# Performance work log

Hardware: AMD Instinct MI355X
Metric: run time of the kernel (lower is better)

The kernel has to match this reference:

```python
import jax, jax.numpy as jnp
import numpy as np

DIM = 2560
HEADS = 64
HEAD_DIM = 40
TEMB = 512
FF = 4 * DIM
B = 1
S = 1248
TXT = 224
EPS = 1e-6


def _ln(x, eps=EPS):
    # LayerNorm over last dim, no affine (elementwise_affine=False)
    m = jnp.mean(x, axis=-1, keepdims=True)
    v = jnp.mean(jnp.square(x - m), axis=-1, keepdims=True)
    return (x - m) * jax.lax.rsqrt(v + eps)


def setup_inputs() -> dict:
    key = jax.random.key(0)
    ks = jax.random.split(key, 10)
    w = 0.02
    return {
        "hidden_states": jax.random.normal(ks[0], (B, S, DIM), jnp.float32),
        "emb": jax.random.normal(ks[1], (B, TEMB), jnp.float32),
        "attention_mask": jnp.zeros((B, 1, S, S), jnp.float32),
        "adaln_w": jax.random.normal(ks[2], (TEMB, 12 * DIM), jnp.float32) * w,
        "adaln_b": jnp.zeros((12 * DIM,), jnp.float32),
        "qkv_w": jax.random.normal(ks[3], (DIM, 3 * DIM), jnp.float32) * w,
        "qkv_b": jnp.zeros((3 * DIM,), jnp.float32),
        "out_w": jax.random.normal(ks[4], (DIM, DIM), jnp.float32) * w,
        "out_b": jnp.zeros((DIM,), jnp.float32),
        "ff1_w": jax.random.normal(ks[5], (DIM, FF), jnp.float32) * w,
        "ff1_b": jnp.zeros((FF,), jnp.float32),
        "ff2_w": jax.random.normal(ks[6], (FF, DIM), jnp.float32) * w,
        "ff2_b": jnp.zeros((DIM,), jnp.float32),
        "text_length": TXT,
    }


def reference(hidden_states, emb, attention_mask, adaln_w, adaln_b, qkv_w, qkv_b,
              out_w, out_b, ff1_w, ff1_b, ff2_w, ff2_b, text_length):
    b, s, d = hidden_states.shape
    t = text_length

    # adaLN: SiLU -> Linear(time_embed_dim, 12*dim), chunk into 12 [B, dim] pieces
    ada = jax.nn.silu(emb) @ adaln_w + adaln_b
    (sh_msa_i, sc_msa_i, g_msa_i, sh_mlp_i, sc_mlp_i, g_mlp_i,
     sh_msa_t, sc_msa_t, g_msa_t, sh_mlp_t, sc_mlp_t, g_mlp_t) = jnp.split(ada, 12, axis=1)

    def mod(x, shift, scale):
        return x * (1.0 + scale[:, None, :]) + shift[:, None, :]

    # --- attention block ---
    ai = _ln(hidden_states)
    ai = jnp.concatenate([mod(ai[:, :t], sh_msa_t, sc_msa_t),
                          mod(ai[:, t:], sh_msa_i, sc_msa_i)], axis=1)

    qkv = ai @ qkv_w + qkv_b                              # [B, S, 3*D]
    q, k, v = jnp.split(qkv, 3, axis=-1)
    q = q.reshape(b, s, HEADS, HEAD_DIM).transpose(0, 2, 1, 3)  # [B, H, S, hd]
    k = k.reshape(b, s, HEADS, HEAD_DIM).transpose(0, 2, 1, 3)
    v = v.reshape(b, s, HEADS, HEAD_DIM).transpose(0, 2, 1, 3)

    q = _ln(q)  # per-head QK layernorm
    k = _ln(k)

    scores = jnp.einsum("bhqd,bhkd->bhqk", q, k) / (HEAD_DIM ** 0.5)
    scores = scores + attention_mask
    probs = jax.nn.softmax(scores, axis=-1)
    ctx = jnp.einsum("bhqk,bhkd->bhqd", probs, v)
    ctx = ctx.transpose(0, 2, 1, 3).reshape(b, s, d)
    attn_out = ctx @ out_w + out_b

    h = jnp.concatenate([hidden_states[:, :t] + g_msa_t[:, None, :] * attn_out[:, :t],
                         hidden_states[:, t:] + g_msa_i[:, None, :] * attn_out[:, t:]], axis=1)

    # --- MLP block ---
    mi = _ln(h)
    mi = jnp.concatenate([mod(mi[:, :t], sh_mlp_t, sc_mlp_t),
                          mod(mi[:, t:], sh_mlp_i, sc_mlp_i)], axis=1)
    mo = jax.nn.gelu(mi @ ff1_w + ff1_b, approximate=True) @ ff2_w + ff2_b

    h = jnp.concatenate([h[:, :t] + g_mlp_t[:, None, :] * mo[:, :t],
                         h[:, t:] + g_mlp_i[:, None, :] * mo[:, t:]], axis=1)
    return h
```

## Files before the change

### kernel.cpp

```cpp
#include <hip/hip_runtime.h>
#include <cstdint>

typedef float f32x4 __attribute__((ext_vector_type(4)));
typedef __bf16 bf16x8 __attribute__((ext_vector_type(8)));
typedef __bf16 bf16x4 __attribute__((ext_vector_type(4)));

#define S_LEN 1248
#define S_PAD 1280
#define DIMD 2560
#define NHEAD 64
#define HDIM 40
#define T3 7680

__device__ __forceinline__ f32x4 mfma16(bf16x8 a, bf16x8 b, f32x4 c) {
  return __builtin_amdgcn_mfma_f32_16x16x32_bf16(a, b, c, 0, 0, 0);
}

__global__ void k_adaln(const float* __restrict__ emb, const float* __restrict__ W,
                        const float* __restrict__ b, float* __restrict__ ada) {
  __shared__ __attribute__((aligned(16))) float se[512];
  int tid = threadIdx.x;
  for (int i = tid; i < 512; i += 64) {
    float e = emb[i];
    se[i] = e / (1.f + __expf(-e));
  }
  __syncthreads();
  int col = blockIdx.x * 64 + tid;
  float acc = 0.f;
  #pragma unroll 8
  for (int k = 0; k < 512; ++k) acc += se[k] * W[(size_t)k * 30720 + col];
  ada[col] = acc + b[col];
}

__global__ __launch_bounds__(256) void k_trans(const float* __restrict__ W,
                                               __bf16* __restrict__ Wt, int K, int N) {
  __shared__ __attribute__((aligned(16))) float t[64][65];
  int k0 = blockIdx.y * 64, n0 = blockIdx.x * 64;
  int tid = threadIdx.x;
  #pragma unroll
  for (int i = 0; i < 4; ++i) {
    int r = i * 16 + (tid >> 4), c = (tid & 15) * 4;
    const float4 v = *(const float4*)&W[(size_t)(k0 + r) * N + n0 + c];
    t[r][c] = v.x; t[r][c + 1] = v.y; t[r][c + 2] = v.z; t[r][c + 3] = v.w;
  }
  __syncthreads();
  #pragma unroll
  for (int j = 0; j < 4; ++j) {
    int n = j * 16 + (tid >> 4), kk = (tid & 15) * 4;
    bf16x4 o;
    o[0] = (__bf16)t[kk][n];     o[1] = (__bf16)t[kk + 1][n];
    o[2] = (__bf16)t[kk + 2][n]; o[3] = (__bf16)t[kk + 3][n];
    *(bf16x4*)&Wt[(size_t)(n0 + n) * K + k0 + kk] = o;
  }
}

__global__ __launch_bounds__(256) void k_lnmod(const float* __restrict__ X,
                                               const float* __restrict__ ada,
                                               int csh_t, int csc_t, int csh_i, int csc_i,
                                               const int* __restrict__ tlp,
                                               __bf16* __restrict__ Y) {
  int row = blockIdx.x, tid = threadIdx.x;
  const float* x = X + (size_t)row * DIMD;
  float v[10], s = 0.f, s2 = 0.f;
  #pragma unroll
  for (int i = 0; i < 10; ++i) { v[i] = x[tid + i * 256]; s += v[i]; s2 += v[i] * v[i]; }
  #pragma unroll
  for (int m = 1; m < 64; m <<= 1) { s += __shfl_xor(s, m, 64); s2 += __shfl_xor(s2, m, 64); }
  __shared__ float rs[4], rq[4];
  if ((tid & 63) == 0) { rs[tid >> 6] = s; rq[tid >> 6] = s2; }
  __syncthreads();
  s = rs[0] + rs[1] + rs[2] + rs[3];
  s2 = rq[0] + rq[1] + rq[2] + rq[3];
  float mean = s * (1.f / DIMD);
  float rstd = rsqrtf(s2 * (1.f / DIMD) - mean * mean + 1e-6f);
  int txt = *tlp;
  int csh = row < txt ? csh_t : csh_i, csc = row < txt ? csc_t : csc_i;
  #pragma unroll
  for (int i = 0; i < 10; ++i) {
    int col = tid + i * 256;
    float y = (v[i] - mean) * rstd;
    y = y * (1.f + ada[csc * DIMD + col]) + ada[csh * DIMD + col];
    Y[(size_t)row * DIMD + col] = (__bf16)y;
  }
}

template <int EPI>
__global__ __launch_bounds__(256) void k_gemm(
    const __bf16* __restrict__ A, int lda, const __bf16* __restrict__ Bt, int ldb,
    const float* __restrict__ bias, int N, int ksize,
    float* __restrict__ Cf, float* __restrict__ Cp, __bf16* __restrict__ Cb) {
  __shared__ __attribute__((aligned(16))) __bf16 smem[3][2][4096];
  int tid = threadIdx.x;

  unsigned gx = gridDim.x, gy = gridDim.y;
  unsigned nwg = gx * gy * gridDim.z;
  unsigned orig = (blockIdx.z * gy + blockIdx.y) * gx + blockIdx.x;
  unsigned qq = nwg >> 3, r8 = nwg & 7;
  unsigned xcd = orig & 7, loc = orig >> 3;
  unsigned swz = (xcd < r8 ? xcd * (qq + 1) : r8 * (qq + 1) + (xcd - r8) * qq) + loc;
  unsigned bx = swz % gx;
  unsigned rest = swz / gx;
  unsigned by = rest % gy;
  unsigned bz = rest / gy;

  int m0 = bx * 128, n0 = by * 128;
  int kbase = bz * ksize;
  int wave = tid >> 6, lane = tid & 63;
  int wm = (wave & 1) * 64, wn = (wave >> 1) * 64;
  int l15 = lane & 15, l4 = lane >> 4;
  f32x4 acc[4][4] = {};

  auto STG = [&](__bf16* As, __bf16* Bs, int kk) {
    #pragma unroll
    for (int i = 0; i < 2; ++i) {
      int c = tid + i * 256;
      int row = c >> 2, ko = (c & 3) * 8;
      __builtin_amdgcn_global_load_lds(
          (const __attribute__((address_space(1))) unsigned int*)(A + (size_t)(m0 + row) * lda + kk + ko),
          (__attribute__((address_space(3))) unsigned int*)(As + c * 8), 16, 0, 0);
      __builtin_amdgcn_global_load_lds(
          (const __attribute__((address_space(1))) unsigned int*)(Bt + (size_t)(n0 + row) * ldb + kk + ko),
          (__attribute__((address_space(3))) unsigned int*)(Bs + c * 8), 16, 0, 0);
    }
  };

  int nt = ksize >> 5;
  STG(smem[0][0], smem[0][1], kbase);
  STG(smem[1][0], smem[1][1], kbase + 32);
  asm volatile("s_waitcnt vmcnt(4)" ::: "memory");
  __builtin_amdgcn_s_barrier();

  int rb = 0, sb = 2;
  for (int t = 0; t < nt; ++t) {
    if (t + 2 < nt) STG(smem[sb][0], smem[sb][1], kbase + (t + 2) * 32);
    const __bf16* As = smem[rb][0];
    const __bf16* Bs = smem[rb][1];
    bf16x8 af[4], bfr[4];
    #pragma unroll
    for (int s = 0; s < 4; ++s) {
      af[s] = *(const bf16x8*)&As[(wm + s * 16 + l15) * 32 + l4 * 8];
      bfr[s] = *(const bf16x8*)&Bs[(wn + s * 16 + l15) * 32 + l4 * 8];
    }
    __builtin_amdgcn_s_setprio(1);
    #pragma unroll
    for (int i = 0; i < 4; ++i)
      #pragma unroll
      for (int j = 0; j < 4; ++j)
        acc[i][j] = mfma16(af[i], bfr[j], acc[i][j]);
    __builtin_amdgcn_s_setprio(0);
    __builtin_amdgcn_sched_barrier(0);
    if (t + 2 < nt)
      asm volatile("s_waitcnt vmcnt(4)" ::: "memory");
    else
      asm volatile("s_waitcnt vmcnt(0)" ::: "memory");
    __builtin_amdgcn_s_barrier();
    rb = rb == 2 ? 0 : rb + 1;
    sb = sb == 2 ? 0 : sb + 1;
  }

  float* Cfo = Cf;
  if constexpr (EPI == 3) Cfo = (bz == 0) ? Cf : (Cp + (size_t)(bz - 1) * S_PAD * N);
  #pragma unroll
  for (int i = 0; i < 4; ++i) {
    #pragma unroll
    for (int r = 0; r < 4; ++r) {
      int rr = m0 + wm + i * 16 + l4 * 4 + r;
      if (rr >= S_LEN) continue;
      #pragma unroll
      for (int j = 0; j < 4; ++j) {
        int col = n0 + wn + j * 16 + l15;
        if constexpr (EPI == 0) {
          Cfo[(size_t)rr * N + col] = acc[i][j][r] + bias[col];
        } else if constexpr (EPI == 3) {
          Cfo[(size_t)rr * N + col] = acc[i][j][r];
        } else if constexpr (EPI == 4) {
          Cb[(size_t)rr * N + col] = (__bf16)(acc[i][j][r] + bias[col]);
        } else {
          float val = acc[i][j][r] + bias[col];
          float u = val + 0.044715f * val * val * val;
          float gl = 0.5f * val * (1.f + tanhf(0.7978845608028654f * u));
          Cb[(size_t)rr * N + col] = (__bf16)gl;
        }
      }
    }
  }
}

template <int NS>
__global__ __launch_bounds__(256) void k_red(const float* __restrict__ p0,
                                             const float* __restrict__ prest,
                                             const float* __restrict__ bias,
                                             const float* __restrict__ resid,
                                             const float* __restrict__ ada,
                                             int g_t, int g_i, const int* __restrict__ tlp,
                                             int N, float* __restrict__ out) {
  int idx = blockIdx.x * 256 + threadIdx.x;
  int perRow = N >> 2;
  int row = idx / perRow;
  int c4 = (idx - row * perRow) << 2;
  if (row >= S_LEN) return;
  int txt = *tlp;
  size_t off = (size_t)row * N + c4;
  float4 s = *(const float4*)&p0[off];
  #pragma unroll
  for (int z = 0; z < NS - 1; ++z) {
    const float4 p = *(const float4*)&prest[(size_t)z * S_PAD * N + off];
    s.x += p.x; s.y += p.y; s.z += p.z; s.w += p.w;
  }
  const float4 bb = *(const float4*)&bias[c4];
  const float4 rr = *(const float4*)&resid[off];
  const float4 gg = *(const float4*)&ada[(size_t)(row < txt ? g_t : g_i) * DIMD + c4];
  float4 o;
  o.x = rr.x + gg.x * (s.x + bb.x);
  o.y = rr.y + gg.y * (s.y + bb.y);
  o.z = rr.z + gg.z * (s.z + bb.z);
  o.w = rr.w + gg.w * (s.w + bb.w);
  *(float4*)&out[off] = o;
}

__global__ __launch_bounds__(128) void k_qkln(const __bf16* __restrict__ qkv,
                                              __bf16* __restrict__ Qb, __bf16* __restrict__ Kb) {
  __shared__ __attribute__((aligned(16))) float buf[5120];
  int srow = blockIdx.x, tid = threadIdx.x;
  const __bf16* rowp = qkv + (size_t)srow * T3;
  for (int i = tid; i < 640; i += 128) {
    bf16x8 v = *(const bf16x8*)&rowp[i * 8];
    #pragma unroll
    for (int j = 0; j < 8; ++j) buf[i * 8 + j] = (float)v[j];
  }
  __syncthreads();
  int h = tid & 63;
  bool isK = tid >= 64;
  const float* x = buf + (isK ? DIMD : 0) + h * HDIM;
  float xv[40], s = 0.f;
  #pragma unroll
  for (int d = 0; d < 40; ++d) { xv[d] = x[d]; s += xv[d]; }
  float mean = s * (1.f / 40.f);
  float s2 = 0.f;
  #pragma unroll
  for (int d = 0; d < 40; ++d) { float t = xv[d] - mean; s2 += t * t; }
  float rstd = rsqrtf(s2 * (1.f / 40.f) + 1e-6f);
  float scale = isK ? rstd : rstd * 0.15811388300841897f;
  __bf16* dst = (isK ? Kb : Qb) + ((size_t)h * S_PAD + srow) * 64;
  #pragma unroll
  for (int i = 0; i < 5; ++i) {
    bf16x8 w;
    #pragma unroll
    for (int j = 0; j < 8; ++j) w[j] = (__bf16)((xv[i * 8 + j] - mean) * scale);
    *(bf16x8*)&dst[i * 8] = w;
  }
  bf16x8 z = {};
  *(bf16x8*)&dst[40] = z;
  *(bf16x8*)&dst[48] = z;
  *(bf16x8*)&dst[56] = z;
}

__global__ __launch_bounds__(256) void k_vtrans(const __bf16* __restrict__ qkv,
                                                __bf16* __restrict__ Vt) {
  __shared__ __attribute__((aligned(16))) float t[64][41];
  int h = blockIdx.y, s0 = blockIdx.x * 64;
  int tid = threadIdx.x;
  for (int i = tid; i < 64 * 40; i += 256) {
    int sr = i / 40, d = i - sr * 40;
    int srow = s0 + sr;
    t[sr][d] = (srow < S_LEN) ? (float)qkv[(size_t)srow * T3 + 2 * DIMD + h * HDIM + d] : 0.f;
  }
  __syncthreads();
  int d = tid >> 2, sc = (tid & 3) * 16;
  bf16x8 w0 = {}, w1 = {};
  if (d < 40) {
    #pragma unroll
    for (int q = 0; q < 8; ++q) {
      w0[q] = (__bf16)t[sc + q][d];
      w1[q] = (__bf16)t[sc + 8 + q][d];
    }
  } else if (d == 40) {
    #pragma unroll
    for (int q = 0; q < 8; ++q) { w0[q] = (__bf16)1.0f; w1[q] = (__bf16)1.0f; }
  }
  __bf16* dst = Vt + ((size_t)h * 64 + d) * S_PAD + s0 + sc;
  *(bf16x8*)&dst[0] = w0;
  *(bf16x8*)&dst[8] = w1;
}

__global__ __launch_bounds__(256) void k_attn(const __bf16* __restrict__ Qb,
                                              const __bf16* __restrict__ Kb,
                                              const __bf16* __restrict__ Vt,
                                              const float* __restrict__ mask,
                                              __bf16* __restrict__ ctx) {
  __shared__ __attribute__((aligned(16))) __bf16 kvs[2][2][4096];
  __shared__ __attribute__((aligned(16))) __bf16 plds[4][2][1024];
  unsigned orig = blockIdx.y * 10 + blockIdx.x;
  unsigned swz = (orig & 7) * 80 + (orig >> 3);
  int h = swz / 10, q0 = (swz % 10) * 128;
  int tid = threadIdx.x, wave = tid >> 6, lane = tid & 63;
  int l15 = lane & 15, l4 = lane >> 4;
  int qb = q0 + wave * 32;

  const __bf16* Kh = Kb + (size_t)h * S_PAD * 64;
  const __bf16* Vh = Vt + (size_t)h * 64 * S_PAD;

  auto STAGE = [&](int buf, int kv0) {
    #pragma unroll
    for (int i = 0; i < 2; ++i) {
      int c = tid + i * 256;
      int row = c >> 3, col = ((c & 7) ^ (row & 7)) * 8;
      __builtin_amdgcn_global_load_lds(
          (const __attribute__((address_space(1))) unsigned int*)(Kh + (size_t)(kv0 + row) * 64 + col),
          (__attribute__((address_space(3))) unsigned int*)&kvs[buf][0][c * 8], 16, 0, 0);
      __builtin_amdgcn_global_load_lds(
          (const __attribute__((address_space(1))) unsigned int*)(Vh + (size_t)row * S_PAD + kv0 + col),
          (__attribute__((address_space(3))) unsigned int*)&kvs[buf][1][c * 8], 16, 0, 0);
    }
  };

  bf16x8 qf[2][2];
  #pragma unroll
  for (int g = 0; g < 2; ++g) {
    const __bf16* Qp = Qb + ((size_t)h * S_PAD + qb + g * 16 + l15) * 64 + l4 * 8;
    qf[g][0] = *(const bf16x8*)Qp;
    qf[g][1] = *(const bf16x8*)(Qp + 32);
  }
  const float* mrow[2][4];
  #pragma unroll
  for (int g = 0; g < 2; ++g)
    #pragma unroll
    for (int r = 0; r < 4; ++r) {
      int qr = qb + g * 16 + l4 * 4 + r;
      mrow[g][r] = mask + (size_t)(qr < S_LEN ? qr : S_LEN - 1) * S_LEN;
    }
  f32x4 o[2][3] = {};

  STAGE(0, 0);
  for (int t = 0; t < 20; ++t) {
    int kv0 = t * 64;
    if (t < 19) {
      STAGE((t + 1) & 1, kv0 + 64);
      asm volatile("s_waitcnt vmcnt(4)" ::: "memory");
    } else {
      asm volatile("s_waitcnt vmcnt(0)" ::: "memory");
    }
    __builtin_amdgcn_s_barrier();
    const __bf16* Ks = kvs[t & 1][0];
    const __bf16* Vs = kvs[t & 1][1];

    float mreg[2][4][4];
    #pragma unroll
    for (int g = 0; g < 2; ++g)
      #pragma unroll
      for (int ns = 0; ns < 4; ++ns) {
        int kvc = kv0 + ns * 16 + l15;
        int mc = kvc < S_LEN ? kvc : S_LEN - 1;
        #pragma unroll
        for (int r = 0; r < 4; ++r) mreg[g][ns][r] = mrow[g][r][mc];
      }

    bf16x8 kf[4][2];
    #pragma unroll
    for (int ns = 0; ns < 4; ++ns) {
      int kvr = ns * 16 + l15, sw = kvr & 7;
      kf[ns][0] = *(const bf16x8*)((const char*)Ks + kvr * 128 + ((l4 ^ sw) << 4));
      kf[ns][1] = *(const bf16x8*)((const char*)Ks + kvr * 128 + (((4 + l4) ^ sw) << 4));
    }
    bf16x8 vf[3][2];
    #pragma unroll
    for (int d3 = 0; d3 < 3; ++d3) {
      int dr = d3 * 16 + l15, sw = dr & 7;
      vf[d3][0] = *(const bf16x8*)((const char*)Vs + dr * 128 + ((l4 ^ sw) << 4));
      vf[d3][1] = *(const bf16x8*)((const char*)Vs + dr * 128 + (((4 + l4) ^ sw) << 4));
    }

    #pragma unroll
    for (int g = 0; g < 2; ++g) {
      f32x4 sf[4];
      #pragma unroll
      for (int ns = 0; ns < 4; ++ns) {
        f32x4 a = {};
        a = mfma16(qf[g][0], kf[ns][0], a);
        a = mfma16(qf[g][1], kf[ns][1], a);
        sf[ns] = a;
      }
      #pragma unroll
      for (int ns = 0; ns < 4; ++ns) {
        int kvc = kv0 + ns * 16 + l15;
        #pragma unroll
        for (int r = 0; r < 4; ++r) {
          float val = sf[ns][r] - 8.f + mreg[g][ns][r];
          if (kvc >= S_LEN) val = -100.f;
          float e = __expf(val);
          int prow = l4 * 4 + r;
          int boff = (prow * 128 + (ns * 16 + l15) * 2) ^ ((prow & 7) << 4);
          plds[wave][g][boff >> 1] = (__bf16)e;
        }
      }
      int swp = (l15 & 7) << 4;
      int ba = l15 * 128 + l4 * 16;
      bf16x8 pa0 = *(const bf16x8*)((const char*)plds[wave][g] + (ba ^ swp));
      bf16x8 pa1 = *(const bf16x8*)((const char*)plds[wave][g] + ((ba + 64) ^ swp));
      #pragma unroll
      for (int d3 = 0; d3 < 3; ++d3) {
        o[g][d3] = mfma16(pa0, vf[d3][0], o[g][d3]);
        o[g][d3] = mfma16(pa1, vf[d3][1], o[g][d3]);
      }
    }
    __builtin_amdgcn_s_barrier();
  }

  #pragma unroll
  for (int g = 0; g < 2; ++g) {
    #pragma unroll
    for (int r = 0; r < 4; ++r) {
      float sum = __shfl(o[g][2][r], (lane & 0x30) + 8, 64);
      float rinv = 1.f / sum;
      int qr = qb + g * 16 + l4 * 4 + r;
      if (qr < S_LEN) {
        #pragma unroll
        for (int d3 = 0; d3 < 3; ++d3) {
          int d = d3 * 16 + l15;
          if (d < HDIM)
            ctx[(size_t)qr * DIMD + h * HDIM + d] = (__bf16)(o[g][d3][r] * rinv);
        }
      }
    }
  }
}

extern "C" void kernel_launch(void* const* d_in, const int* in_sizes, int n_in,
                              void* d_out, int out_size, void* d_ws, size_t ws_size,
                              hipStream_t stream) {
  const float* hidden  = (const float*)d_in[0];
  const float* emb     = (const float*)d_in[1];
  const float* mask    = (const float*)d_in[2];
  const float* adaln_w = (const float*)d_in[3];
  const float* adaln_b = (const float*)d_in[4];
  const float* qkv_w   = (const float*)d_in[5];
  const float* qkv_b   = (const float*)d_in[6];
  const float* out_w   = (const float*)d_in[7];
  const float* out_b   = (const float*)d_in[8];
  const float* ff1_w   = (const float*)d_in[9];
  const float* ff1_b   = (const float*)d_in[10];
  const float* ff2_w   = (const float*)d_in[11];
  const float* ff2_b   = (const float*)d_in[12];
  const int*   tl      = (const int*)d_in[13];
  (void)in_sizes; (void)n_in; (void)out_size; (void)ws_size;

  char* w = (char*)d_ws;
  size_t off = 0;
  auto alloc = [&](size_t b) { char* p = w + off; off += (b + 255) & ~(size_t)255; return p; };
  float*  ada  = (float*)alloc(30720 * 4);
  __bf16* wT   = (__bf16*)alloc((size_t)10240 * 2560 * 2);
  __bf16* ai   = (__bf16*)alloc((size_t)S_PAD * DIMD * 2);
  __bf16* actB = (__bf16*)alloc((size_t)S_PAD * 10240 * 2);
  __bf16* Qb   = (__bf16*)alloc((size_t)NHEAD * S_PAD * 64 * 2);
  __bf16* Kb   = (__bf16*)alloc((size_t)NHEAD * S_PAD * 64 * 2);
  __bf16* Vt   = (__bf16*)alloc((size_t)NHEAD * 64 * S_PAD * 2);
  __bf16* ctxb = (__bf16*)alloc((size_t)S_PAD * DIMD * 2);
  float*  hbuf = (float*)alloc((size_t)S_PAD * DIMD * 4);
  __bf16* mi    = ai;
  __bf16* qkvB  = actB;
  __bf16* ff1o  = actB;
  float*  partO = (float*)Qb;
  float*  partF = (float*)Qb;

  k_adaln<<<dim3(480), dim3(64), 0, stream>>>(emb, adaln_w, adaln_b, ada);
  k_lnmod<<<dim3(1248), dim3(256), 0, stream>>>(hidden, ada, 6, 7, 0, 1, tl, ai);
  k_trans<<<dim3(7680 / 64, 2560 / 64), dim3(256), 0, stream>>>(qkv_w, wT, 2560, 7680);
  k_gemm<4><<<dim3(10, 60, 1), dim3(256), 0, stream>>>(ai, 2560, wT, 2560, qkv_b, 7680, 2560,
                                                       nullptr, nullptr, qkvB);
  k_qkln<<<dim3(1248), dim3(128), 0, stream>>>(qkvB, Qb, Kb);
  k_vtrans<<<dim3(20, 64), dim3(256), 0, stream>>>(qkvB, Vt);
  k_attn<<<dim3(10, 64), dim3(256), 0, stream>>>(Qb, Kb, Vt, mask, ctxb);
  k_trans<<<dim3(2560 / 64, 2560 / 64), dim3(256), 0, stream>>>(out_w, wT, 2560, 2560);
  k_gemm<3><<<dim3(10, 20, 2), dim3(256), 0, stream>>>(ctxb, 2560, wT, 2560, nullptr, 2560, 1280,
                                                       partO, partO + (size_t)S_PAD * 2560, nullptr);
  k_red<2><<<dim3(3120), dim3(256), 0, stream>>>(partO, partO + (size_t)S_PAD * 2560, out_b,
                                                 hidden, ada, 8, 2, tl, 2560, hbuf);
  k_lnmod<<<dim3(1248), dim3(256), 0, stream>>>(hbuf, ada, 9, 10, 3, 4, tl, mi);
  k_trans<<<dim3(10240 / 64, 2560 / 64), dim3(256), 0, stream>>>(ff1_w, wT, 2560, 10240);
  k_gemm<2><<<dim3(10, 80, 1), dim3(256), 0, stream>>>(mi, 2560, wT, 2560, ff1_b, 10240, 2560,
                                                       nullptr, nullptr, ff1o);
  k_trans<<<dim3(2560 / 64, 10240 / 64), dim3(256), 0, stream>>>(ff2_w, wT, 10240, 2560);
  k_gemm<3><<<dim3(10, 20, 2), dim3(256), 0, stream>>>(ff1o, 10240, wT, 10240, nullptr, 2560, 5120,
                                                       partF, partF + (size_t)S_PAD * 2560, nullptr);
  k_red<2><<<dim3(3120), dim3(256), 0, stream>>>(partF, partF + (size_t)S_PAD * 2560, ff2_b,
                                                 hbuf, ada, 11, 5, tl, 2560, (float*)d_out);
}
```

Before: 557.0 us.

## Fuse weight transposes into neighbouring kernels to overlap with compute

Moves each fp32-to-bf16 weight transpose into the grid of an earlier, independent kernel. The QKV transpose joins the first layernorm, the out-proj transpose joins the QKV GEMM, the FF1 transpose joins attention, and the FF2 transpose joins the out-proj GEMM, with blocks split by block index. The aim is to hide the memory-bound transposes behind compute-bound GEMM and attention work and to cut kernel launches. This needs separate transposed-weight buffers, one of which reuses hbuf. Every fused kernel now allocates the largest shared-memory footprint of its two parts, which can lower occupancy for the transpose blocks.

```diff
diff --git a/kernel.cpp b/kernel.cpp
--- a/kernel.cpp
+++ b/kernel.cpp
@@ -16,26 +16,12 @@
   return __builtin_amdgcn_mfma_f32_16x16x32_bf16(a, b, c, 0, 0, 0);
 }
 
-__global__ void k_adaln(const float* __restrict__ emb, const float* __restrict__ W,
-                        const float* __restrict__ b, float* __restrict__ ada) {
-  __shared__ __attribute__((aligned(16))) float se[512];
-  int tid = threadIdx.x;
-  for (int i = tid; i < 512; i += 64) {
-    float e = emb[i];
-    se[i] = e / (1.f + __expf(-e));
-  }
-  __syncthreads();
-  int col = blockIdx.x * 64 + tid;
-  float acc = 0.f;
-  #pragma unroll 8
-  for (int k = 0; k < 512; ++k) acc += se[k] * W[(size_t)k * 30720 + col];
-  ada[col] = acc + b[col];
-}
-
-__global__ __launch_bounds__(256) void k_trans(const float* __restrict__ W,
-                                               __bf16* __restrict__ Wt, int K, int N) {
-  __shared__ __attribute__((aligned(16))) float t[64][65];
-  int k0 = blockIdx.y * 64, n0 = blockIdx.x * 64;
+
+__device__ __forceinline__ void dev_trans(int vbid, const float* __restrict__ W,
+                                          __bf16* __restrict__ Wt, int K, int N, char* smraw) {
+  float (*t)[65] = (float(*)[65])smraw;
+  int gxt = N >> 6;
+  int n0 = (vbid % gxt) * 64, k0 = (vbid / gxt) * 64;
   int tid = threadIdx.x;
   #pragma unroll
   for (int i = 0; i < 4; ++i) {
@@ -54,19 +40,20 @@
   }
 }
 
-__global__ __launch_bounds__(256) void k_lnmod(const float* __restrict__ X,
-                                               const float* __restrict__ ada,
-                                               int csh_t, int csc_t, int csh_i, int csc_i,
-                                               const int* __restrict__ tlp,
-                                               __bf16* __restrict__ Y) {
-  int row = blockIdx.x, tid = threadIdx.x;
+__device__ __forceinline__ void dev_lnmod(int row, const float* __restrict__ X,
+                                          const float* __restrict__ ada,
+                                          int csh_t, int csc_t, int csh_i, int csc_i,
+                                          const int* __restrict__ tlp,
+                                          __bf16* __restrict__ Y, char* smraw) {
+  float* rs = (float*)smraw;
+  float* rq = rs + 4;
+  int tid = threadIdx.x;
   const float* x = X + (size_t)row * DIMD;
   float v[10], s = 0.f, s2 = 0.f;
   #pragma unroll
   for (int i = 0; i < 10; ++i) { v[i] = x[tid + i * 256]; s += v[i]; s2 += v[i] * v[i]; }
   #pragma unroll
   for (int m = 1; m < 64; m <<= 1) { s += __shfl_xor(s, m, 64); s2 += __shfl_xor(s2, m, 64); }
-  __shared__ float rs[4], rq[4];
   if ((tid & 63) == 0) { rs[tid >> 6] = s; rq[tid >> 6] = s2; }
   __syncthreads();
   s = rs[0] + rs[1] + rs[2] + rs[3];
@@ -85,16 +72,17 @@
 }
 
 template <int EPI>
-__global__ __launch_bounds__(256) void k_gemm(
-    const __bf16* __restrict__ A, int lda, const __bf16* __restrict__ Bt, int ldb,
-    const float* __restrict__ bias, int N, int ksize,
-    float* __restrict__ Cf, float* __restrict__ Cp, __bf16* __restrict__ Cb) {
-  __shared__ __attribute__((aligned(16))) __bf16 smem[3][2][4096];
+__device__ __forceinline__ void dev_gemm(int vbid, unsigned gx, unsigned gy, unsigned gz,
+                                         const __bf16* __restrict__ A, int lda,
+                                         const __bf16* __restrict__ Bt, int ldb,
+                                         const float* __restrict__ bias, int N, int ksize,
+                                         float* __restrict__ Cf, float* __restrict__ Cp,
+                                         __bf16* __restrict__ Cb, char* smraw) {
+  __bf16 (*smem)[2][4096] = (__bf16(*)[2][4096])smraw;
   int tid = threadIdx.x;
 
-  unsigned gx = gridDim.x, gy = gridDim.y;
-  unsigned nwg = gx * gy * gridDim.z;
-  unsigned orig = (blockIdx.z * gy + blockIdx.y) * gx + blockIdx.x;
+  unsigned nwg = gx * gy * gz;
+  unsigned orig = (unsigned)vbid;
   unsigned qq = nwg >> 3, r8 = nwg & 7;
   unsigned xcd = orig & 7, loc = orig >> 3;
   unsigned swz = (xcd < r8 ? xcd * (qq + 1) : r8 * (qq + 1) + (xcd - r8) * qq) + loc;
@@ -186,111 +174,13 @@
   }
 }
 
-template <int NS>
-__global__ __launch_bounds__(256) void k_red(const float* __restrict__ p0,
-                                             const float* __restrict__ prest,
-                                             const float* __restrict__ bias,
-                                             const float* __restrict__ resid,
-                                             const float* __restrict__ ada,
-                                             int g_t, int g_i, const int* __restrict__ tlp,
-                                             int N, float* __restrict__ out) {
-  int idx = blockIdx.x * 256 + threadIdx.x;
-  int perRow = N >> 2;
-  int row = idx / perRow;
-  int c4 = (idx - row * perRow) << 2;
-  if (row >= S_LEN) return;
-  int txt = *tlp;
-  size_t off = (size_t)row * N + c4;
-  float4 s = *(const float4*)&p0[off];
-  #pragma unroll
-  for (int z = 0; z < NS - 1; ++z) {
-    const float4 p = *(const float4*)&prest[(size_t)z * S_PAD * N + off];
-    s.x += p.x; s.y += p.y; s.z += p.z; s.w += p.w;
-  }
-  const float4 bb = *(const float4*)&bias[c4];
-  const float4 rr = *(const float4*)&resid[off];
-  const float4 gg = *(const float4*)&ada[(size_t)(row < txt ? g_t : g_i) * DIMD + c4];
-  float4 o;
-  o.x = rr.x + gg.x * (s.x + bb.x);
-  o.y = rr.y + gg.y * (s.y + bb.y);
-  o.z = rr.z + gg.z * (s.z + bb.z);
-  o.w = rr.w + gg.w * (s.w + bb.w);
-  *(float4*)&out[off] = o;
-}
-
-__global__ __launch_bounds__(128) void k_qkln(const __bf16* __restrict__ qkv,
-                                              __bf16* __restrict__ Qb, __bf16* __restrict__ Kb) {
-  __shared__ __attribute__((aligned(16))) float buf[5120];
-  int srow = blockIdx.x, tid = threadIdx.x;
-  const __bf16* rowp = qkv + (size_t)srow * T3;
-  for (int i = tid; i < 640; i += 128) {
-    bf16x8 v = *(const bf16x8*)&rowp[i * 8];
-    #pragma unroll
-    for (int j = 0; j < 8; ++j) buf[i * 8 + j] = (float)v[j];
-  }
-  __syncthreads();
-  int h = tid & 63;
-  bool isK = tid >= 64;
-  const float* x = buf + (isK ? DIMD : 0) + h * HDIM;
-  float xv[40], s = 0.f;
-  #pragma unroll
-  for (int d = 0; d < 40; ++d) { xv[d] = x[d]; s += xv[d]; }
-  float mean = s * (1.f / 40.f);
-  float s2 = 0.f;
-  #pragma unroll
-  for (int d = 0; d < 40; ++d) { float t = xv[d] - mean; s2 += t * t; }
-  float rstd = rsqrtf(s2 * (1.f / 40.f) + 1e-6f);
-  float scale = isK ? rstd : rstd * 0.15811388300841897f;
-  __bf16* dst = (isK ? Kb : Qb) + ((size_t)h * S_PAD + srow) * 64;
-  #pragma unroll
-  for (int i = 0; i < 5; ++i) {
-    bf16x8 w;
-    #pragma unroll
-    for (int j = 0; j < 8; ++j) w[j] = (__bf16)((xv[i * 8 + j] - mean) * scale);
-    *(bf16x8*)&dst[i * 8] = w;
-  }
-  bf16x8 z = {};
-  *(bf16x8*)&dst[40] = z;
-  *(bf16x8*)&dst[48] = z;
-  *(bf16x8*)&dst[56] = z;
-}
-
-__global__ __launch_bounds__(256) void k_vtrans(const __bf16* __restrict__ qkv,
-                                                __bf16* __restrict__ Vt) {
-  __shared__ __attribute__((aligned(16))) float t[64][41];
-  int h = blockIdx.y, s0 = blockIdx.x * 64;
-  int tid = threadIdx.x;
-  for (int i = tid; i < 64 * 40; i += 256) {
-    int sr = i / 40, d = i - sr * 40;
-    int srow = s0 + sr;
-    t[sr][d] = (srow < S_LEN) ? (float)qkv[(size_t)srow * T3 + 2 * DIMD + h * HDIM + d] : 0.f;
-  }
-  __syncthreads();
-  int d = tid >> 2, sc = (tid & 3) * 16;
-  bf16x8 w0 = {}, w1 = {};
-  if (d < 40) {
-    #pragma unroll
-    for (int q = 0; q < 8; ++q) {
-      w0[q] = (__bf16)t[sc + q][d];
-      w1[q] = (__bf16)t[sc + 8 + q][d];
-    }
-  } else if (d == 40) {
-    #pragma unroll
-    for (int q = 0; q < 8; ++q) { w0[q] = (__bf16)1.0f; w1[q] = (__bf16)1.0f; }
-  }
-  __bf16* dst = Vt + ((size_t)h * 64 + d) * S_PAD + s0 + sc;
-  *(bf16x8*)&dst[0] = w0;
-  *(bf16x8*)&dst[8] = w1;
-}
-
-__global__ __launch_bounds__(256) void k_attn(const __bf16* __restrict__ Qb,
-                                              const __bf16* __restrict__ Kb,
-                                              const __bf16* __restrict__ Vt,
-                                              const float* __restrict__ mask,
-                                              __bf16* __restrict__ ctx) {
-  __shared__ __attribute__((aligned(16))) __bf16 kvs[2][2][4096];
-  __shared__ __attribute__((aligned(16))) __bf16 plds[4][2][1024];
-  unsigned orig = blockIdx.y * 10 + blockIdx.x;
+__device__ void dev_attn(int vbid, const __bf16* __restrict__ Qb,
+                         const __bf16* __restrict__ Kb, const __bf16* __restrict__ Vt,
+                         const float* __restrict__ mask, __bf16* __restrict__ ctx,
+                         char* smraw) {
+  __bf16 (*kvs)[2][4096] = (__bf16(*)[2][4096])smraw;
+  __bf16 (*plds)[2][1024] = (__bf16(*)[2][1024])(smraw + 32768);
+  unsigned orig = (unsigned)vbid;
   unsigned swz = (orig & 7) * 80 + (orig >> 3);
   int h = swz / 10, q0 = (swz % 10) * 128;
   int tid = threadIdx.x, wave = tid >> 6, lane = tid & 63;
@@ -425,6 +315,179 @@
   }
 }
 
+
+__global__ void k_adaln(const float* __restrict__ emb, const float* __restrict__ W,
+                        const float* __restrict__ b, float* __restrict__ ada) {
+  __shared__ __attribute__((aligned(16))) float se[512];
+  int tid = threadIdx.x;
+  for (int i = tid; i < 512; i += 64) {
+    float e = emb[i];
+    se[i] = e / (1.f + __expf(-e));
+  }
+  __syncthreads();
+  int col = blockIdx.x * 64 + tid;
+  float acc = 0.f;
+  #pragma unroll 8
+  for (int k = 0; k < 512; ++k) acc += se[k] * W[(size_t)k * 30720 + col];
+  ada[col] = acc + b[col];
+}
+
+__global__ __launch_bounds__(256) void k_lnmod_qtrans(const float* __restrict__ X,
+                                                      const float* __restrict__ ada,
+                                                      const int* __restrict__ tlp,
+                                                      __bf16* __restrict__ Y,
+                                                      const float* __restrict__ W,
+                                                      __bf16* __restrict__ Wt) {
+  __shared__ __attribute__((aligned(16))) char sm[16640];
+  int b = blockIdx.x;
+  if (b < 1248) dev_lnmod(b, X, ada, 6, 7, 0, 1, tlp, Y, sm);
+  else dev_trans(b - 1248, W, Wt, 2560, 7680, sm);
+}
+
+__global__ __launch_bounds__(256) void k_lnmod(const float* __restrict__ X,
+                                               const float* __restrict__ ada,
+                                               int csh_t, int csc_t, int csh_i, int csc_i,
+                                               const int* __restrict__ tlp,
+                                               __bf16* __restrict__ Y) {
+  __shared__ __attribute__((aligned(16))) char sm[64];
+  dev_lnmod(blockIdx.x, X, ada, csh_t, csc_t, csh_i, csc_i, tlp, Y, sm);
+}
+
+template <int EPI>
+__global__ __launch_bounds__(256) void k_gemm_trans(
+    const __bf16* __restrict__ A, int lda, const __bf16* __restrict__ Bt, int ldb,
+    const float* __restrict__ bias, int N, int ksize,
+    float* __restrict__ Cf, float* __restrict__ Cp, __bf16* __restrict__ Cb,
+    unsigned gx, unsigned gy, unsigned gz,
+    const float* __restrict__ W, __bf16* __restrict__ Wt, int tK, int tN) {
+  __shared__ __attribute__((aligned(16))) char sm[49152];
+  int b = blockIdx.x;
+  int split = (int)(gx * gy * gz);
+  if (b < split) dev_gemm<EPI>(b, gx, gy, gz, A, lda, Bt, ldb, bias, N, ksize, Cf, Cp, Cb, sm);
+  else dev_trans(b - split, W, Wt, tK, tN, sm);
+}
+
+template <int EPI>
+__global__ __launch_bounds__(256) void k_gemm(
+    const __bf16* __restrict__ A, int lda, const __bf16* __restrict__ Bt, int ldb,
+    const float* __restrict__ bias, int N, int ksize,
+    float* __restrict__ Cf, float* __restrict__ Cp, __bf16* __restrict__ Cb) {
+  __shared__ __attribute__((aligned(16))) char sm[49152];
+  int vbid = (blockIdx.z * gridDim.y + blockIdx.y) * gridDim.x + blockIdx.x;
+  dev_gemm<EPI>(vbid, gridDim.x, gridDim.y, gridDim.z, A, lda, Bt, ldb, bias, N, ksize,
+                Cf, Cp, Cb, sm);
+}
+
+__global__ __launch_bounds__(256) void k_attn_trans(const __bf16* __restrict__ Qb,
+                                                    const __bf16* __restrict__ Kb,
+                                                    const __bf16* __restrict__ Vt,
+                                                    const float* __restrict__ mask,
+                                                    __bf16* __restrict__ ctx,
+                                                    const float* __restrict__ W,
+                                                    __bf16* __restrict__ Wt, int tK, int tN) {
+  __shared__ __attribute__((aligned(16))) char sm[49152];
+  int b = blockIdx.x;
+  if (b < 640) dev_attn(b, Qb, Kb, Vt, mask, ctx, sm);
+  else dev_trans(b - 640, W, Wt, tK, tN, sm);
+}
+
+template <int NS>
+__global__ __launch_bounds__(256) void k_red(const float* __restrict__ p0,
+                                             const float* __restrict__ prest,
+                                             const float* __restrict__ bias,
+                                             const float* __restrict__ resid,
+                                             const float* __restrict__ ada,
+                                             int g_t, int g_i, const int* __restrict__ tlp,
+                                             int N, float* __restrict__ out) {
+  int idx = blockIdx.x * 256 + threadIdx.x;
+  int perRow = N >> 2;
+  int row = idx / perRow;
+  int c4 = (idx - row * perRow) << 2;
+  if (row >= S_LEN) return;
+  int txt = *tlp;
+  size_t off = (size_t)row * N + c4;
+  float4 s = *(const float4*)&p0[off];
+  #pragma unroll
+  for (int z = 0; z < NS - 1; ++z) {
+    const float4 p = *(const float4*)&prest[(size_t)z * S_PAD * N + off];
+    s.x += p.x; s.y += p.y; s.z += p.z; s.w += p.w;
+  }
+  const float4 bb = *(const float4*)&bias[c4];
+  const float4 rr = *(const float4*)&resid[off];
+  const float4 gg = *(const float4*)&ada[(size_t)(row < txt ? g_t : g_i) * DIMD + c4];
+  float4 o;
+  o.x = rr.x + gg.x * (s.x + bb.x);
+  o.y = rr.y + gg.y * (s.y + bb.y);
+  o.z = rr.z + gg.z * (s.z + bb.z);
+  o.w = rr.w + gg.w * (s.w + bb.w);
+  *(float4*)&out[off] = o;
+}
+
+__global__ __launch_bounds__(128) void k_qkln(const __bf16* __restrict__ qkv,
+                                              __bf16* __restrict__ Qb, __bf16* __restrict__ Kb) {
+  __shared__ __attribute__((aligned(16))) float buf[5120];
+  int srow = blockIdx.x, tid = threadIdx.x;
+  const __bf16* rowp = qkv + (size_t)srow * T3;
+  for (int i = tid; i < 640; i += 128) {
+    bf16x8 v = *(const bf16x8*)&rowp[i * 8];
+    #pragma unroll
+    for (int j = 0; j < 8; ++j) buf[i * 8 + j] = (float)v[j];
+  }
+  __syncthreads();
+  int h = tid & 63;
+  bool isK = tid >= 64;
+  const float* x = buf + (isK ? DIMD : 0) + h * HDIM;
+  float xv[40], s = 0.f;
+  #pragma unroll
+  for (int d = 0; d < 40; ++d) { xv[d] = x[d]; s += xv[d]; }
+  float mean = s * (1.f / 40.f);
+  float s2 = 0.f;
+  #pragma unroll
+  for (int d = 0; d < 40; ++d) { float t = xv[d] - mean; s2 += t * t; }
+  float rstd = rsqrtf(s2 * (1.f / 40.f) + 1e-6f);
+  float scale = isK ? rstd : rstd * 0.15811388300841897f;
+  __bf16* dst = (isK ? Kb : Qb) + ((size_t)h * S_PAD + srow) * 64;
+  #pragma unroll
+  for (int i = 0; i < 5; ++i) {
+    bf16x8 w;
+    #pragma unroll
+    for (int j = 0; j < 8; ++j) w[j] = (__bf16)((xv[i * 8 + j] - mean) * scale);
+    *(bf16x8*)&dst[i * 8] = w;
+  }
+  bf16x8 z = {};
+  *(bf16x8*)&dst[40] = z;
+  *(bf16x8*)&dst[48] = z;
+  *(bf16x8*)&dst[56] = z;
+}
+
+__global__ __launch_bounds__(256) void k_vtrans(const __bf16* __restrict__ qkv,
+                                                __bf16* __restrict__ Vt) {
+  __shared__ __attribute__((aligned(16))) float t[64][41];
+  int h = blockIdx.y, s0 = blockIdx.x * 64;
+  int tid = threadIdx.x;
+  for (int i = tid; i < 64 * 40; i += 256) {
+    int sr = i / 40, d = i - sr * 40;
+    int srow = s0 + sr;
+    t[sr][d] = (srow < S_LEN) ? (float)qkv[(size_t)srow * T3 + 2 * DIMD + h * HDIM + d] : 0.f;
+  }
+  __syncthreads();
+  int d = tid >> 2, sc = (tid & 3) * 16;
+  bf16x8 w0 = {}, w1 = {};
+  if (d < 40) {
+    #pragma unroll
+    for (int q = 0; q < 8; ++q) {
+      w0[q] = (__bf16)t[sc + q][d];
+      w1[q] = (__bf16)t[sc + 8 + q][d];
+    }
+  } else if (d == 40) {
+    #pragma unroll
+    for (int q = 0; q < 8; ++q) { w0[q] = (__bf16)1.0f; w1[q] = (__bf16)1.0f; }
+  }
+  __bf16* dst = Vt + ((size_t)h * 64 + d) * S_PAD + s0 + sc;
+  *(bf16x8*)&dst[0] = w0;
+  *(bf16x8*)&dst[8] = w1;
+}
+
 extern "C" void kernel_launch(void* const* d_in, const int* in_sizes, int n_in,
                               void* d_out, int out_size, void* d_ws, size_t ws_size,
                               hipStream_t stream) {
@@ -448,7 +511,8 @@
   size_t off = 0;
   auto alloc = [&](size_t b) { char* p = w + off; off += (b + 255) & ~(size_t)255; return p; };
   float*  ada  = (float*)alloc(30720 * 4);
-  __bf16* wT   = (__bf16*)alloc((size_t)10240 * 2560 * 2);
+  __bf16* wTf1 = (__bf16*)alloc((size_t)10240 * 2560 * 2);
+  __bf16* wTq2 = (__bf16*)alloc((size_t)10240 * 2560 * 2);
   __bf16* ai   = (__bf16*)alloc((size_t)S_PAD * DIMD * 2);
   __bf16* actB = (__bf16*)alloc((size_t)S_PAD * 10240 * 2);
   __bf16* Qb   = (__bf16*)alloc((size_t)NHEAD * S_PAD * 64 * 2);
@@ -459,28 +523,28 @@
   __bf16* mi    = ai;
   __bf16* qkvB  = actB;
   __bf16* ff1o  = actB;
+  __bf16* wTo   = (__bf16*)hbuf;
   float*  partO = (float*)Qb;
   float*  partF = (float*)Qb;
 
   k_adaln<<<dim3(480), dim3(64), 0, stream>>>(emb, adaln_w, adaln_b, ada);
-  k_lnmod<<<dim3(1248), dim3(256), 0, stream>>>(hidden, ada, 6, 7, 0, 1, tl, ai);
-  k_trans<<<dim3(7680 / 64, 2560 / 64), dim3(256), 0, stream>>>(qkv_w, wT, 2560, 7680);
-  k_gemm<4><<<dim3(10, 60, 1), dim3(256), 0, stream>>>(ai, 2560, wT, 2560, qkv_b, 7680, 2560,
-                                                       nullptr, nullptr, qkvB);
+  k_lnmod_qtrans<<<dim3(1248 + 4800), dim3(256), 0, stream>>>(hidden, ada, tl, ai, qkv_w, wTq2);
+  k_gemm_trans<4><<<dim3(600 + 1600), dim3(256), 0, stream>>>(
+      ai, 2560, wTq2, 2560, qkv_b, 7680, 2560, nullptr, nullptr, qkvB,
+      10, 60, 1, out_w, wTo, 2560, 2560);
   k_qkln<<<dim3(1248), dim3(128), 0, stream>>>(qkvB, Qb, Kb);
   k_vtrans<<<dim3(20, 64), dim3(256), 0, stream>>>(qkvB, Vt);
-  k_attn<<<dim3(10, 64), dim3(256), 0, stream>>>(Qb, Kb, Vt, mask, ctxb);
-  k_trans<<<dim3(2560 / 64, 2560 / 64), dim3(256), 0, stream>>>(out_w, wT, 2560, 2560);
-  k_gemm<3><<<dim3(10, 20, 2), dim3(256), 0, stream>>>(ctxb, 2560, wT, 2560, nullptr, 2560, 1280,
-                                                       partO, partO + (size_t)S_PAD * 2560, nullptr);
+  k_attn_trans<<<dim3(640 + 6400), dim3(256), 0, stream>>>(Qb, Kb, Vt, mask, ctxb,
+                                                           ff1_w, wTf1, 2560, 10240);
+  k_gemm_trans<3><<<dim3(400 + 6400), dim3(256), 0, stream>>>(
+      ctxb, 2560, wTo, 2560, nullptr, 2560, 1280, partO, partO + (size_t)S_PAD * 2560, nullptr,
+      10, 20, 2, ff2_w, wTq2, 10240, 2560);
   k_red<2><<<dim3(3120), dim3(256), 0, stream>>>(partO, partO + (size_t)S_PAD * 2560, out_b,
                                                  hidden, ada, 8, 2, tl, 2560, hbuf);
   k_lnmod<<<dim3(1248), dim3(256), 0, stream>>>(hbuf, ada, 9, 10, 3, 4, tl, mi);
-  k_trans<<<dim3(10240 / 64, 2560 / 64), dim3(256), 0, stream>>>(ff1_w, wT, 2560, 10240);
-  k_gemm<2><<<dim3(10, 80, 1), dim3(256), 0, stream>>>(mi, 2560, wT, 2560, ff1_b, 10240, 2560,
+  k_gemm<2><<<dim3(10, 80, 1), dim3(256), 0, stream>>>(mi, 2560, wTf1, 2560, ff1_b, 10240, 2560,
                                                        nullptr, nullptr, ff1o);
-  k_trans<<<dim3(2560 / 64, 10240 / 64), dim3(256), 0, stream>>>(ff2_w, wT, 10240, 2560);
-  k_gemm<3><<<dim3(10, 20, 2), dim3(256), 0, stream>>>(ff1o, 10240, wT, 10240, nullptr, 2560, 5120,
+  k_gemm<3><<<dim3(10, 20, 2), dim3(256), 0, stream>>>(ff1o, 10240, wTq2, 10240, nullptr, 2560, 5120,
                                                        partF, partF + (size_t)S_PAD * 2560, nullptr);
   k_red<2><<<dim3(3120), dim3(256), 0, stream>>>(partF, partF + (size_t)S_PAD * 2560, ff2_b,
                                                  hbuf, ada, 11, 5, tl, 2560, (float*)d_out);
```

New measurement: 540.9 us. -2.9%, faster.
